# Kernel optimization log

Measured on AMD Instinct MI355X. Metric: run time of the kernel, lower is better.

## Reference

```python
import jax, jax.numpy as jnp
import numpy as np

D_MODEL = 1024
N_HEADS = 16
D_K = D_MODEL // N_HEADS  # 64
THETA = 10000.0


def _rope(x, token_positions):
    # x: [b, h, s, d], token_positions: [s]
    inv_freq = 1.0 / THETA ** (jnp.arange(0, D_K, 2, dtype=jnp.float32) / D_K)  # [d/2]
    ang = token_positions.astype(jnp.float32)[:, None] * inv_freq               # [s, d/2]
    cos, sin = jnp.cos(ang), jnp.sin(ang)                                       # broadcast over b,h
    x1 = x[..., 0::2]
    x2 = x[..., 1::2]
    even = x1 * cos - x2 * sin
    odd = x1 * sin + x2 * cos
    return jnp.stack([even, odd], axis=-1).reshape(x.shape)  # re-interleave


def setup_inputs() -> dict:
    key = jax.random.key(0)
    k1, k2, k3 = jax.random.split(key, 3)
    B, S = 2, 2048
    x = jax.random.normal(k1, (B, S, D_MODEL), dtype=jnp.float32)
    token_positions = jnp.arange(S, dtype=jnp.int32)
    std_qkv = np.sqrt(2.0 / (D_MODEL + 3 * D_MODEL))
    std_out = np.sqrt(2.0 / (D_MODEL + D_MODEL))
    W_qkv = jax.random.normal(k2, (3 * D_MODEL, D_MODEL), dtype=jnp.float32) * std_qkv
    W_out = jax.random.normal(k3, (D_MODEL, D_MODEL), dtype=jnp.float32) * std_out
    return {"x": x, "token_positions": token_positions, "W_qkv": W_qkv, "W_out": W_out}


def reference(x, token_positions, W_qkv, W_out):
    B, S, _ = x.shape
    qkv = jnp.einsum('bsi,oi->bso', x, W_qkv)                 # [b, s, 3*h*d]
    qkv = qkv.reshape(B, S, 3, N_HEADS, D_K)
    qkv = jnp.transpose(qkv, (2, 0, 3, 1, 4))                 # [3, b, h, s, d]
    q, k, v = qkv[0], qkv[1], qkv[2]
    q = _rope(q, token_positions)
    k = _rope(k, token_positions)
    scores = jnp.einsum('bhqd,bhkd->bhqk', q, k) / jnp.sqrt(jnp.float32(D_K))
    mask = jnp.tril(jnp.ones((S, S), dtype=bool))
    scores = jnp.where(mask, scores, -jnp.inf)
    attn = jax.nn.softmax(scores, axis=-1)
    out = jnp.einsum('bhqk,bhkd->bhqd', attn, v)              # [b, h, s, d]
    out = jnp.transpose(out, (0, 2, 1, 3)).reshape(B, S, D_MODEL)
    return jnp.einsum('bsi,oi->bso', out, W_out)
```

## Files before the change

### kernel.cpp

```cpp
#include <hip/hip_runtime.h>
#include <hip/hip_bf16.h>
#include <math.h>

#define D_MODEL 1024
#define N_HEADS 16
#define D_K     64
#define S_LEN   2048
#define B_SZ    2

typedef unsigned short u16;
typedef unsigned int   u32;
using short8 = __attribute__((ext_vector_type(8))) short;
using f32x4  = __attribute__((ext_vector_type(4))) float;

__device__ inline float bf2f(u16 u) { return __uint_as_float((u32)u << 16); }
__device__ inline u16 f2bf(float f) {
    __hip_bfloat16 h = __float2bfloat16(f);
    return *(u16*)&h;
}
__device__ inline void gload_lds16(const void* g, void* l) {
    __builtin_amdgcn_global_load_lds(
        (const __attribute__((address_space(1))) unsigned int*)g,
        (__attribute__((address_space(3))) unsigned int*)l, 16, 0, 0);
}

__global__ __launch_bounds__(256)
void cast3_f32_bf16(const float* __restrict__ a, u16* __restrict__ ao, int na4,
                    const float* __restrict__ bsrc, u16* __restrict__ bo, int nb4,
                    const float* __restrict__ c, u16* __restrict__ co, int nc4) {
    int j = blockIdx.x * 256 + threadIdx.x;
    const float* src; u16* dst;
    if (j < na4) { src = a; dst = ao; }
    else {
        j -= na4;
        if (j < nb4) { src = bsrc; dst = bo; }
        else {
            j -= nb4;
            if (j >= nc4) return;
            src = c; dst = co;
        }
    }
    float4 v = ((const float4*)src)[j];
    ushort4 u;
    u.x = f2bf(v.x); u.y = f2bf(v.y); u.z = f2bf(v.z); u.w = f2bf(v.w);
    ((ushort4*)dst)[j] = u;
}

template <bool OUT_BF16>
__global__ __launch_bounds__(256)
void gemm_bt_mfma(const u16* __restrict__ A, const u16* __restrict__ B,
                  void* __restrict__ Cout, int M, int N, int K) {
    __shared__ u16 As[128 * 32];
    __shared__ u16 Bs[128 * 32];
    const int tid  = threadIdx.x;
    const int lane = tid & 63;
    const int wv   = tid >> 6;
    const int wm   = wv >> 1, wn = wv & 1;
    const int row0 = blockIdx.y * 128;
    const int col0 = blockIdx.x * 128;

    const int lr = lane >> 2;
    const int lc = (lane & 3) * 8;

    f32x4 acc[4][4] = {};

    for (int k0 = 0; k0 < K; k0 += 32) {
#pragma unroll
        for (int t = 0; t < 2; t++) {
            int rblk = wv * 32 + t * 16;
            gload_lds16(A + (size_t)(row0 + rblk + lr) * K + k0 + lc, &As[rblk * 32]);
            gload_lds16(B + (size_t)(col0 + rblk + lr) * K + k0 + lc, &Bs[rblk * 32]);
        }
        __syncthreads();

        short8 af[4], bfr[4];
#pragma unroll
        for (int mi = 0; mi < 4; mi++)
            af[mi] = *(const short8*)&As[(wm * 64 + mi * 16 + (lane & 15)) * 32 + (lane >> 4) * 8];
#pragma unroll
        for (int nj = 0; nj < 4; nj++)
            bfr[nj] = *(const short8*)&Bs[(wn * 64 + nj * 16 + (lane & 15)) * 32 + (lane >> 4) * 8];
#pragma unroll
        for (int mi = 0; mi < 4; mi++)
#pragma unroll
            for (int nj = 0; nj < 4; nj++)
                acc[mi][nj] = __builtin_amdgcn_mfma_f32_16x16x32_bf16(
                    af[mi], bfr[nj], acc[mi][nj], 0, 0, 0);
        __syncthreads();
    }

    const int cr = (lane >> 4) * 4;
    const int cc = lane & 15;
#pragma unroll
    for (int mi = 0; mi < 4; mi++) {
#pragma unroll
        for (int nj = 0; nj < 4; nj++) {
            int c = col0 + wn * 64 + nj * 16 + cc;
#pragma unroll
            for (int r = 0; r < 4; r++) {
                int rr = row0 + wm * 64 + mi * 16 + cr + r;
                if (OUT_BF16)
                    ((u16*)Cout)[(size_t)rr * N + c] = f2bf(acc[mi][nj][r]);
                else
                    ((float*)Cout)[(size_t)rr * N + c] = acc[mi][nj][r];
            }
        }
    }
}

__global__ __launch_bounds__(256)
void rope_bf16(u16* __restrict__ qkv, const int* __restrict__ pos) {
    int idx = blockIdx.x * blockDim.x + threadIdx.x;
    int j = idx & 31;
    int h = (idx >> 5) & 15;
    int w = (idx >> 9) & 1;
    int s = (idx >> 10) & 2047;
    int b = idx >> 21;

    float p = (float)pos[s];
    float inv_freq = __powf(10000.0f, -(float)(2 * j) / 64.0f);
    float ang = p * inv_freq;
    float sn, cs;
    sincosf(ang, &sn, &cs);
    float sc = (w == 0) ? 0.125f : 1.0f;

    size_t base = (((size_t)(b * S_LEN + s) * 3 + w) * D_MODEL) + h * D_K + 2 * j;
    float x1 = bf2f(qkv[base]);
    float x2 = bf2f(qkv[base + 1]);
    qkv[base]     = f2bf((x1 * cs - x2 * sn) * sc);
    qkv[base + 1] = f2bf((x1 * sn + x2 * cs) * sc);
}

__global__ __launch_bounds__(256)
void vtrans(const u16* __restrict__ qkv, u16* __restrict__ VT) {
    __shared__ u16 t[64][68];
    const int st = blockIdx.x, h = blockIdx.y, b = blockIdx.z;
    const int tid = threadIdx.x;
    const int bh = b * N_HEADS + h;

#pragma unroll
    for (int i = 0; i < 4; i++) {
        int e  = tid + i * 256;
        int sl = e >> 4;
        int c4 = e & 15;
        ushort4 v = *(const ushort4*)&qkv[((size_t)(b * S_LEN + st * 64 + sl) * 3 + 2) * D_MODEL
                                          + h * D_K + c4 * 4];
        *(ushort4*)&t[sl][c4 * 4] = v;
    }
    __syncthreads();
#pragma unroll
    for (int i = 0; i < 4; i++) {
        int e  = tid + i * 256;
        int d  = e >> 4;
        int s4 = e & 15;
        ushort4 o;
        o.x = t[s4 * 4 + 0][d];
        o.y = t[s4 * 4 + 1][d];
        o.z = t[s4 * 4 + 2][d];
        o.w = t[s4 * 4 + 3][d];
        *(ushort4*)&VT[((size_t)bh * D_K + d) * S_LEN + st * 64 + s4 * 4] = o;
    }
}

__device__ __forceinline__ void attn_step(
    const u16* __restrict__ Ksc, const u16* __restrict__ Vsc,
    u16* __restrict__ Psw,
    short8 (&qf)[2], f32x4 (&acc)[4], float& mq, float& lq,
    int k0, int qw0, bool diag, int l15, int quad)
{
    f32x4 s[4] = {};
    __builtin_amdgcn_s_setprio(1);
#pragma unroll
    for (int kf = 0; kf < 2; kf++)
#pragma unroll
        for (int nj = 0; nj < 4; nj++) {
            short8 kfr = *(const short8*)&Ksc[kf * 2048 + (nj * 16 + l15) * 32 + quad * 8];
            s[nj] = __builtin_amdgcn_mfma_f32_16x16x32_bf16(kfr, qf[kf], s[nj], 0, 0, 0);
        }
    __builtin_amdgcn_s_setprio(0);

    if (diag) {
        const int row_g = qw0 + l15;
#pragma unroll
        for (int nj = 0; nj < 4; nj++)
#pragma unroll
            for (int r = 0; r < 4; r++) {
                int key_g = k0 + nj * 16 + quad * 4 + r;
                if (key_g > row_g) s[nj][r] = -INFINITY;
            }
    }

    float rmax = s[0][0];
#pragma unroll
    for (int nj = 0; nj < 4; nj++)
#pragma unroll
        for (int r = 0; r < 4; r++) rmax = fmaxf(rmax, s[nj][r]);
    rmax = fmaxf(rmax, __shfl_xor(rmax, 16, 64));
    rmax = fmaxf(rmax, __shfl_xor(rmax, 32, 64));
    float mn = fmaxf(mq, rmax);
    float alpha = __expf(mq - mn);
    mq = mn;
    float rsum = 0.f;
#pragma unroll
    for (int nj = 0; nj < 4; nj++)
#pragma unroll
        for (int r = 0; r < 4; r++) {
            float p = __expf(s[nj][r] - mn);
            s[nj][r] = p;
            rsum += p;
        }
    rsum += __shfl_xor(rsum, 16, 64);
    rsum += __shfl_xor(rsum, 32, 64);
    lq = lq * alpha + rsum;

#pragma unroll
    for (int r = 0; r < 4; r++) {
        float ar = __shfl(alpha, quad * 4 + r, 64);
#pragma unroll
        for (int nj = 0; nj < 4; nj++) acc[nj][r] *= ar;
    }

#pragma unroll
    for (int nj = 0; nj < 4; nj++) {
        u32 lo = ((u32)f2bf(s[nj][1]) << 16) | f2bf(s[nj][0]);
        u32 hi = ((u32)f2bf(s[nj][3]) << 16) | f2bf(s[nj][2]);
        uint2 pk; pk.x = lo; pk.y = hi;
        *(uint2*)&Psw[l15 * 68 + nj * 16 + quad * 4] = pk;
    }

    __builtin_amdgcn_s_setprio(1);
#pragma unroll
    for (int kf = 0; kf < 2; kf++) {
        const u16* pp = &Psw[l15 * 68 + kf * 32 + quad * 8];
        uint2 plo = *(const uint2*)pp;
        uint2 phi = *(const uint2*)(pp + 4);
        u32 praw[4] = { plo.x, plo.y, phi.x, phi.y };
        short8 pf = *(const short8*)praw;
#pragma unroll
        for (int nj = 0; nj < 4; nj++) {
            short8 vf = *(const short8*)&Vsc[kf * 2048 + (nj * 16 + l15) * 32 + quad * 8];
            acc[nj] = __builtin_amdgcn_mfma_f32_16x16x32_bf16(pf, vf, acc[nj], 0, 0, 0);
        }
    }
    __builtin_amdgcn_s_setprio(0);
}

__global__ __launch_bounds__(256)
void attn_mfma(const u16* __restrict__ qkv, const u16* __restrict__ VT,
               u16* __restrict__ out) {
    __shared__ u16 Ks[2][2][64 * 32];
    __shared__ u16 VsT[2][2][64 * 32];
    __shared__ u16 Ps[2][4][16 * 68];

    const int tid  = threadIdx.x;
    const int lane = tid & 63;
    const int wv   = tid >> 6;

    const int bid = blockIdx.x;
    const int idx = bid >> 3;
    const int bh  = (bid & 7) * 4 + (idx >> 4);
    const int pr  = idx & 15;
    const int qtH = 31 - pr;
    const int qtL = pr;
    const int h   = bh & (N_HEADS - 1);
    const int b   = bh >> 4;

    const int l15  = lane & 15;
    const int quad = lane >> 4;
    const int qw0H = qtH * 64 + wv * 16;
    const int qw0L = qtL * 64 + wv * 16;

    const size_t vtb = (size_t)bh * D_K * S_LEN;
    u16* PswH = &Ps[0][wv][0];
    u16* PswL = &Ps[1][wv][0];

    const int lr = lane >> 2;
    const int lc = (lane & 3) * 8;

    short8 qfH[2], qfL[2];
#pragma unroll
    for (int kf = 0; kf < 2; kf++) {
        qfH[kf] = *(const short8*)&qkv[((size_t)(b * S_LEN + qw0H + l15) * 3 + 0) * D_MODEL
                                       + h * D_K + kf * 32 + quad * 8];
        qfL[kf] = *(const short8*)&qkv[((size_t)(b * S_LEN + qw0L + l15) * 3 + 0) * D_MODEL
                                       + h * D_K + kf * 32 + quad * 8];
    }

    f32x4 accH[4] = {}, accL[4] = {};
    float mqH = -INFINITY, lqH = 0.f;
    float mqL = -INFINITY, lqL = 0.f;

    auto STAGE = [&](int kts, int bf) {
        const int k0s = kts * 64;
#pragma unroll
        for (int kf = 0; kf < 2; kf++)
            gload_lds16(qkv + ((size_t)(b * S_LEN + k0s + wv * 16 + lr) * 3 + 1) * D_MODEL
                            + h * D_K + kf * 32 + lc,
                        &Ks[bf][kf][(wv * 16) * 32]);
#pragma unroll
        for (int kc = 0; kc < 2; kc++)
            gload_lds16(VT + vtb + (size_t)(wv * 16 + lr) * S_LEN + k0s + kc * 32 + lc,
                        &VsT[bf][kc][(wv * 16) * 32]);
    };

    STAGE(0, 0);
    __syncthreads();

    int cur = 0;
    for (int kt = 0; kt <= qtH; kt++) {
        const int k0 = kt * 64;

        if (kt < qtH) STAGE(kt + 1, cur ^ 1);

        const u16* Ksc = &Ks[cur][0][0];
        const u16* Vsc = &VsT[cur][0][0];

        attn_step(Ksc, Vsc, PswH, qfH, accH, mqH, lqH,
                  k0, qw0H, kt == qtH, l15, quad);
        if (kt <= qtL)
            attn_step(Ksc, Vsc, PswL, qfL, accL, mqL, lqL,
                      k0, qw0L, kt == qtL, l15, quad);

        __syncthreads();
        cur ^= 1;
    }

    float invlH = 1.f / lqH;
    float invlL = 1.f / lqL;
#pragma unroll
    for (int r = 0; r < 4; r++) {
        float irH = __shfl(invlH, quad * 4 + r, 64);
        float irL = __shfl(invlL, quad * 4 + r, 64);
        int rgH = qw0H + quad * 4 + r;
        int rgL = qw0L + quad * 4 + r;
#pragma unroll
        for (int nj = 0; nj < 4; nj++) {
            out[(size_t)(b * S_LEN + rgH) * D_MODEL + h * D_K + nj * 16 + l15] =
                f2bf(accH[nj][r] * irH);
            out[(size_t)(b * S_LEN + rgL) * D_MODEL + h * D_K + nj * 16 + l15] =
                f2bf(accL[nj][r] * irL);
        }
    }
}

extern "C" void kernel_launch(void* const* d_in, const int* in_sizes, int n_in,
                              void* d_out, int out_size, void* d_ws, size_t ws_size,
                              hipStream_t stream) {
    const float* x    = (const float*)d_in[0];
    const int*   pos  = (const int*)d_in[1];
    const float* Wqkv = (const float*)d_in[2];
    const float* Wout = (const float*)d_in[3];
    float*       out  = (float*)d_out;

    const int M = B_SZ * S_LEN;

    u16* qkvb = (u16*)d_ws;
    u16* aob  = qkvb + (size_t)M * 3 * D_MODEL;
    u16* xb   = aob  + (size_t)M * D_MODEL;
    u16* wqb  = xb   + (size_t)M * D_MODEL;
    u16* wob  = wqb  + (size_t)3 * D_MODEL * D_MODEL;
    u16* vtb  = wob  + (size_t)D_MODEL * D_MODEL;

    const int na4 = M * D_MODEL / 4;
    const int nb4 = 3 * D_MODEL * D_MODEL / 4;
    const int nc4 = D_MODEL * D_MODEL / 4;
    cast3_f32_bf16<<<(na4 + nb4 + nc4 + 255) / 256, 256, 0, stream>>>(
        x, xb, na4, Wqkv, wqb, nb4, Wout, wob, nc4);

    gemm_bt_mfma<true><<<dim3(3 * D_MODEL / 128, M / 128), 256, 0, stream>>>(
        xb, wqb, qkvb, M, 3 * D_MODEL, D_MODEL);

    rope_bf16<<<(B_SZ * S_LEN * 2 * N_HEADS * 32) / 256, 256, 0, stream>>>(qkvb, pos);

    vtrans<<<dim3(S_LEN / 64, N_HEADS, B_SZ), 256, 0, stream>>>(qkvb, vtb);

    attn_mfma<<<(S_LEN / 64) * N_HEADS * B_SZ / 2, 256, 0, stream>>>(qkvb, vtb, aob);

    gemm_bt_mfma<false><<<dim3(D_MODEL / 128, M / 128), 256, 0, stream>>>(
        aob, wob, out, M, D_MODEL, D_MODEL);
}
```

Measured before the change: 222.3 us.

## Skip softmax rescale when max grows little and transpose PV accumulator layout

Online softmax now rescales the accumulator and running sum only when some row's new block max exceeds the stored max by more than 8, so the exp/multiply rescale is skipped in most iterations. The PV MFMA operands are swapped so each lane holds one query row's outputs; this removes the per-row alpha shuffles and lets each lane write its output as packed 4-element stores. The lazy max can leave exponentials up to e^8 above one, which risks reduced precision in bf16 P and in the accumulators.

```diff
diff --git a/kernel.cpp b/kernel.cpp
--- a/kernel.cpp
+++ b/kernel.cpp
@@ -197,28 +197,30 @@
         for (int r = 0; r < 4; r++) rmax = fmaxf(rmax, s[nj][r]);
     rmax = fmaxf(rmax, __shfl_xor(rmax, 16, 64));
     rmax = fmaxf(rmax, __shfl_xor(rmax, 32, 64));
-    float mn = fmaxf(mq, rmax);
-    float alpha = __expf(mq - mn);
-    mq = mn;
+
+    if (!__all(rmax <= mq + 8.f)) {
+        float mn = fmaxf(mq, rmax);
+        float alpha = __expf(mq - mn);
+        mq = mn;
+        lq *= alpha;
+#pragma unroll
+        for (int nj = 0; nj < 4; nj++)
+#pragma unroll
+            for (int r = 0; r < 4; r++) acc[nj][r] *= alpha;
+    }
+
     float rsum = 0.f;
 #pragma unroll
     for (int nj = 0; nj < 4; nj++)
 #pragma unroll
         for (int r = 0; r < 4; r++) {
-            float p = __expf(s[nj][r] - mn);
+            float p = __expf(s[nj][r] - mq);
             s[nj][r] = p;
             rsum += p;
         }
     rsum += __shfl_xor(rsum, 16, 64);
     rsum += __shfl_xor(rsum, 32, 64);
-    lq = lq * alpha + rsum;
-
-#pragma unroll
-    for (int r = 0; r < 4; r++) {
-        float ar = __shfl(alpha, quad * 4 + r, 64);
-#pragma unroll
-        for (int nj = 0; nj < 4; nj++) acc[nj][r] *= ar;
-    }
+    lq += rsum;
 
 #pragma unroll
     for (int nj = 0; nj < 4; nj++) {
@@ -239,7 +241,7 @@
 #pragma unroll
         for (int nj = 0; nj < 4; nj++) {
             short8 vf = *(const short8*)&Vsc[kf * 2048 + (nj * 16 + l15) * 32 + quad * 8];
-            acc[nj] = __builtin_amdgcn_mfma_f32_16x16x32_bf16(pf, vf, acc[nj], 0, 0, 0);
+            acc[nj] = __builtin_amdgcn_mfma_f32_16x16x32_bf16(vf, pf, acc[nj], 0, 0, 0);
         }
     }
     __builtin_amdgcn_s_setprio(0);
@@ -328,18 +330,16 @@
     float invlH = 1.f / lqH;
     float invlL = 1.f / lqL;
 #pragma unroll
-    for (int r = 0; r < 4; r++) {
-        float irH = __shfl(invlH, quad * 4 + r, 64);
-        float irL = __shfl(invlL, quad * 4 + r, 64);
-        int rgH = qw0H + quad * 4 + r;
-        int rgL = qw0L + quad * 4 + r;
-#pragma unroll
-        for (int nj = 0; nj < 4; nj++) {
-            out[(size_t)(b * S_LEN + rgH) * D_MODEL + h * D_K + nj * 16 + l15] =
-                f2bf(accH[nj][r] * irH);
-            out[(size_t)(b * S_LEN + rgL) * D_MODEL + h * D_K + nj * 16 + l15] =
-                f2bf(accL[nj][r] * irL);
-        }
+    for (int nj = 0; nj < 4; nj++) {
+        ushort4 oH, oL;
+        oH.x = f2bf(accH[nj][0] * invlH); oH.y = f2bf(accH[nj][1] * invlH);
+        oH.z = f2bf(accH[nj][2] * invlH); oH.w = f2bf(accH[nj][3] * invlH);
+        oL.x = f2bf(accL[nj][0] * invlL); oL.y = f2bf(accL[nj][1] * invlL);
+        oL.z = f2bf(accL[nj][2] * invlL); oL.w = f2bf(accL[nj][3] * invlL);
+        *(ushort4*)&out[(size_t)(b * S_LEN + qw0H + l15) * D_MODEL
+                        + h * D_K + nj * 16 + quad * 4] = oH;
+        *(ushort4*)&out[(size_t)(b * S_LEN + qw0L + l15) * D_MODEL
+                        + h * D_K + nj * 16 + quad * 4] = oL;
     }
 }
 
```

Result: no change. 221.3 us (-0.5%).
